# Performance work log

Hardware: AMD Instinct MI355X
Metric: run time of the kernel (lower is better)

The kernel has to match this reference:

```python
import jax, jax.numpy as jnp
import numpy as np

B, DIM, H, W, NH, WS = 128, 768, 16, 16, 12, 16
N = H * W  # 256, equals window_size**2


def setup_inputs() -> dict:
    key = jax.random.key(0)
    ks = jax.random.split(key, 8)
    s = 0.02  # small init scale for params
    return {
        "x": jax.random.normal(ks[0], (B, DIM, H, W), dtype=jnp.float32),
        "face_priors": jax.random.uniform(ks[1], (B, N, N), dtype=jnp.float32),
        "qkv_w": jax.random.normal(ks[2], (3 * DIM, DIM), dtype=jnp.float32) * s,
        "qkv_b": jax.random.normal(ks[3], (3 * DIM,), dtype=jnp.float32) * s,
        "rel_table": jax.random.normal(ks[4], ((2 * WS - 1) * (2 * WS - 1), NH), dtype=jnp.float32) * s,
        "face_prior": jax.random.normal(ks[5], (1, NH, N, N), dtype=jnp.float32) * s,
        "proj_w": jax.random.normal(ks[6], (DIM, DIM), dtype=jnp.float32) * s,
        "proj_b": jax.random.normal(ks[7], (DIM,), dtype=jnp.float32) * s,
    }


def _relative_position_bias(rel_table, h, w):
    # Static index computation (h, w are Python ints under jit).
    coords = jnp.stack(jnp.meshgrid(jnp.arange(h), jnp.arange(w), indexing="ij"))  # [2,h,w]
    flat = coords.reshape(2, -1)                     # [2, N]
    rel = flat[:, :, None] - flat[:, None, :]        # [2, N, N]
    idx = (rel[0] + h - 1) * (2 * w - 1) + (rel[1] + w - 1)  # [N, N]
    return rel_table[idx].transpose(2, 0, 1)         # [nh, N, N]


def reference(x, face_priors, qkv_w, qkv_b, rel_table, face_prior, proj_w, proj_b):
    b, c, h, w = x.shape
    n = h * w
    nh = face_prior.shape[1]
    hd = c // nh
    scale = hd ** -0.5

    x_flat = x.reshape(b, c, n).transpose(0, 2, 1)   # [B, N, C]
    qkv = (x_flat @ qkv_w.T + qkv_b).reshape(b, n, 3, nh, hd).transpose(2, 0, 3, 1, 4)
    q, k, v = qkv[0], qkv[1], qkv[2]                 # each [B, nh, N, hd]

    attn = jnp.einsum("bhnd,bhmd->bhnm", q, k) * scale
    attn = attn + face_prior + _relative_position_bias(rel_table, h, w)[None]
    attn = attn * face_priors[:, None]               # broadcast over heads
    attn = jax.nn.softmax(attn, axis=-1)

    out = jnp.einsum("bhnm,bhmd->bhnd", attn, v)     # [B, nh, N, hd]
    out = out.transpose(0, 2, 1, 3).reshape(b, n, c)
    out = out @ proj_w.T + proj_b                    # [B, N, C]
    return out.transpose(0, 2, 1).reshape(b, c, h, w)
```

## Files before the change

kernel.cpp:

```cpp
#include <hip/hip_runtime.h>

#define B_   128
#define DIM_ 768
#define NH_  12
#define HD_  64
#define N_   256

using half8 = __attribute__((ext_vector_type(8))) _Float16;
using half4 = __attribute__((ext_vector_type(4))) _Float16;
using f32x4 = __attribute__((ext_vector_type(4))) float;
typedef unsigned short u16;
typedef unsigned int   u32;

#define GLDS16(srcp, dstp) \
    __builtin_amdgcn_global_load_lds( \
        (const __attribute__((address_space(1))) void*)(srcp), \
        (__attribute__((address_space(3))) void*)(dstp), 16, 0, 0)

__device__ __forceinline__ int xcd_chunked(int orig, int nwg) {
    int xcd = orig & 7, loc = orig >> 3;
    int qq = nwg >> 3, rr = nwg & 7;
    return (xcd < rr ? xcd * (qq + 1) : rr * (qq + 1) + (xcd - rr) * qq) + loc;
}

__global__ __launch_bounds__(256) void bias16_kernel(
    const float* __restrict__ face_prior, const float* __restrict__ rel_table,
    _Float16* __restrict__ b16)
{
    int gid = blockIdx.x * 256 + threadIdx.x;
    int idx = gid * 2;
    union { _Float16 s[2]; u32 u; } P;
    #pragma unroll
    for (int j = 0; j < 2; ++j) {
        int id = idx + j;
        int m = id & 255;
        int n = (id >> 8) & 255;
        int h = id >> 16;
        int rn = n >> 4, cn = n & 15;
        int rm = m >> 4, cm = m & 15;
        int ridx = (rn - rm + 15) * 31 + (cn - cm + 15);
        P.s[j] = (_Float16)(face_prior[id] + rel_table[ridx * NH_ + h]);
    }
    *(u32*)(b16 + idx) = P.u;
}

__global__ __launch_bounds__(256) void conv_f32_f16(
    const float* __restrict__ in, _Float16* __restrict__ o16, int n8)
{
    int i = blockIdx.x * 256 + threadIdx.x;
    if (i >= n8) return;
    float4 a = *(const float4*)(in + (size_t)i * 8);
    float4 b = *(const float4*)(in + (size_t)i * 8 + 4);
    float v[8] = {a.x, a.y, a.z, a.w, b.x, b.y, b.z, b.w};
    union { _Float16 s[8]; uint4 q; } H;
    #pragma unroll
    for (int j = 0; j < 8; ++j) H.s[j] = (_Float16)v[j];
    *(uint4*)(o16 + (size_t)i * 8) = H.q;
}

__global__ __launch_bounds__(256) void conv_w_f16_staged(
    const float* __restrict__ in, _Float16* __restrict__ o16, int nchunk)
{
    int gid = blockIdx.x * 256 + threadIdx.x;
    if (gid >= nchunk) return;
    int t   = gid / 12288;
    int rem = gid % 12288;
    int ks  = rem >> 9;
    int c   = rem & 511;
    int mtb = c >> 6, kgrp = (c >> 4) & 3, r16 = c & 15;
    int srow = t * 128 + mtb * 16 + r16;
    int sk   = ks * 32 + kgrp * 8;
    float4 a = *(const float4*)(in + (size_t)srow * DIM_ + sk);
    float4 b = *(const float4*)(in + (size_t)srow * DIM_ + sk + 4);
    float v[8] = {a.x, a.y, a.z, a.w, b.x, b.y, b.z, b.w};
    union { _Float16 s[8]; uint4 q; } H;
    #pragma unroll
    for (int j = 0; j < 8; ++j) H.s[j] = (_Float16)v[j];
    *(uint4*)(o16 + (size_t)gid * 8) = H.q;
}

__global__ __launch_bounds__(256) void conv_qw_staged(
    const float* __restrict__ in, _Float16* __restrict__ o16, int nchunk)
{
    int gid = blockIdx.x * 256 + threadIdx.x;
    if (gid >= nchunk) return;
    int t   = gid / 24576;
    int rem = gid % 24576;
    int ks  = rem >> 10;
    int c   = rem & 1023;
    int mtb = c >> 6, kg = (c >> 4) & 3, r16 = c & 15;
    int srow = t * 256 + mtb * 16 + r16;
    int sk   = ks * 32 + kg * 8;
    float4 a = *(const float4*)(in + (size_t)srow * DIM_ + sk);
    float4 b = *(const float4*)(in + (size_t)srow * DIM_ + sk + 4);
    float v[8] = {a.x, a.y, a.z, a.w, b.x, b.y, b.z, b.w};
    union { _Float16 s[8]; uint4 q; } H;
    #pragma unroll
    for (int j = 0; j < 8; ++j) H.s[j] = (_Float16)v[j];
    *(uint4*)(o16 + (size_t)gid * 8) = H.q;
}

__global__ __launch_bounds__(256) void conv_transpose_x_f16(
    const float* __restrict__ x, _Float16* __restrict__ xa)
{
    __shared__ float T[64][65];
    const int b = blockIdx.z, k0 = blockIdx.x * 64, n0 = blockIdx.y * 64;
    const int t = threadIdx.x;
    const float* xb = x + (size_t)b * DIM_ * N_;
    {
        int nn = t & 63, kg = t >> 6;
        #pragma unroll
        for (int r = 0; r < 16; ++r) {
            int kk = r * 4 + kg;
            T[kk][nn] = xb[(size_t)(k0 + kk) * N_ + n0 + nn];
        }
    }
    __syncthreads();
    {
        int kk2 = (t & 31) * 2, ng = t >> 5;
        #pragma unroll
        for (int r = 0; r < 8; ++r) {
            int nn = r * 8 + ng;
            union { _Float16 s[2]; u32 u; } P;
            P.s[0] = (_Float16)T[kk2][nn];
            P.s[1] = (_Float16)T[kk2 + 1][nn];
            int n = n0 + nn, k = k0 + kk2;
            int ks = k >> 5, kg = (k >> 3) & 3, koff = k & 7;
            int mtb = n >> 4, r16 = n & 15;
            size_t o = (((size_t)b * 24 + ks) * 1024
                        + mtb * 64 + kg * 16 + r16) * 8 + koff;
            *(u32*)(xa + o) = P.u;
        }
    }
}

__global__ __launch_bounds__(512) void qkv_gemm(
    const _Float16* __restrict__ w16, const _Float16* __restrict__ x16,
    const float* __restrict__ bvec,
    _Float16* __restrict__ q16, _Float16* __restrict__ k16,
    _Float16* __restrict__ v16,
    int b0, int cb)
{
    extern __shared__ _Float16 lds[];

    const int tid  = threadIdx.x;
    const int lane = tid & 63;
    const int wv   = tid >> 6;
    const int wr   = wv >> 2;
    const int wc   = wv & 3;

    const int wg = xcd_chunked(blockIdx.x, cb * 9);
    const int by = wg % 9;
    const int bl = wg / 9;
    const int b  = b0 + bl;

    const _Float16* wbase = w16 + (size_t)by * 24 * 8192;
    const _Float16* xbase = x16 + (size_t)b  * 24 * 8192;

    f32x4 acc[8][4];
    #pragma unroll
    for (int i = 0; i < 8; ++i)
        #pragma unroll
        for (int j = 0; j < 4; ++j)
            acc[i][j] = (f32x4){0.f, 0.f, 0.f, 0.f};

    const int sb = wv * 512;

#define SGA(u, s, j) GLDS16(wbase + (size_t)(u) * 16384 + (j) * 4096 + sb + lane * 8, \
                            lds + (s) * 16384 + (j) * 4096 + sb)
#define SGB(u, s, j) GLDS16(xbase + (size_t)(u) * 16384 + (j) * 4096 + sb + lane * 8, \
                            lds + 32768 + (s) * 16384 + (j) * 4096 + sb)

    SGA(0, 0, 0); SGA(0, 0, 1); SGA(0, 0, 2); SGA(0, 0, 3);
    SGB(0, 0, 0); SGB(0, 0, 1); SGB(0, 0, 2); SGB(0, 0, 3);
    SGA(1, 1, 0); SGA(1, 1, 1); SGA(1, 1, 2); SGA(1, 1, 3);
    SGB(1, 1, 0); SGB(1, 1, 1); SGB(1, 1, 2); SGB(1, 1, 3);

    for (int u = 0; u < 12; ++u) {
        const int sl = u & 1;
        if (u < 11) asm volatile("s_waitcnt vmcnt(8)" ::: "memory");
        else        asm volatile("s_waitcnt vmcnt(0)" ::: "memory");
        __builtin_amdgcn_s_barrier();
        __builtin_amdgcn_sched_barrier(0);

        const _Float16* SA = lds + sl * 16384;
        const _Float16* SB = lds + 32768 + sl * 16384;

        half8 af[8][2];
        #pragma unroll
        for (int mt = 0; mt < 8; ++mt) {
            af[mt][0] = *(const half8*)&SA[((wr * 8 + mt) * 64 + lane) * 8];
            af[mt][1] = *(const half8*)&SA[8192 + ((wr * 8 + mt) * 64 + lane) * 8];
        }

        const bool pre = (u + 2 < 12);
        #pragma unroll
        for (int nt = 0; nt < 4; ++nt) {
            if (nt == 1 && pre) { SGA(u + 2, sl, 0); SGA(u + 2, sl, 1); }
            if (nt == 2 && pre) { SGA(u + 2, sl, 2); SGA(u + 2, sl, 3); }
            half8 bf0 = *(const half8*)&SB[((wc * 4 + nt) * 64 + lane) * 8];
            half8 bf1 = *(const half8*)&SB[8192 + ((wc * 4 + nt) * 64 + lane) * 8];
            __builtin_amdgcn_s_setprio(1);
            #pragma unroll
            for (int mt = 0; mt < 8; ++mt) {
                acc[mt][nt] = __builtin_amdgcn_mfma_f32_16x16x32_f16(af[mt][0], bf0, acc[mt][nt], 0, 0, 0);
                acc[mt][nt] = __builtin_amdgcn_mfma_f32_16x16x32_f16(af[mt][1], bf1, acc[mt][nt], 0, 0, 0);
            }
            __builtin_amdgcn_s_setprio(0);
            __builtin_amdgcn_s_barrier();
        }
        if (pre) { SGB(u + 2, sl, 0); SGB(u + 2, sl, 1); SGB(u + 2, sl, 2); SGB(u + 2, sl, 3); }
    }
#undef SGA
#undef SGB

    const int which = by / 3;
    _Float16* slab = (which == 0) ? q16 : (which == 1) ? k16 : v16;
    const int ocr0 = (by % 3) * 256 + wr * 128 + ((lane >> 4) << 2);
    const int nb   = wc * 64 + (lane & 15);

    #pragma unroll
    for (int mt = 0; mt < 8; ++mt) {
        int oc_in = ocr0 + mt * 16;
        float4 bv = *(const float4*)(bvec + which * DIM_ + oc_in);
        int hh = oc_in >> 6, d = oc_in & 63;
        size_t rowbase = ((size_t)bl * NH_ + hh) * (size_t)(N_ * HD_) + d;
        #pragma unroll
        for (int nt = 0; nt < 4; ++nt) {
            int n = nb + nt * 16;
            union { _Float16 s[4]; uint2 u; } H;
            H.s[0] = (_Float16)(acc[mt][nt][0] + bv.x);
            H.s[1] = (_Float16)(acc[mt][nt][1] + bv.y);
            H.s[2] = (_Float16)(acc[mt][nt][2] + bv.z);
            H.s[3] = (_Float16)(acc[mt][nt][3] + bv.w);
            *(uint2*)(slab + rowbase + (size_t)n * HD_) = H.u;
        }
    }
}

__global__ __launch_bounds__(256) void attn_mfma(
    const _Float16* __restrict__ q16, const _Float16* __restrict__ k16,
    const _Float16* __restrict__ v16,
    const _Float16* __restrict__ bias16, const _Float16* __restrict__ fpri16,
    _Float16* __restrict__ ao,
    int b0, int cb)
{
    extern __shared__ _Float16 ldsh[];
    _Float16* KL  = ldsh;
    _Float16* VtL = ldsh + 16384;
    const int tid  = threadIdx.x;
    const int lane = tid & 63;
    const int wv   = tid >> 6;
    _Float16* PL = ldsh + 32768 + wv * 512;

    const int bh = xcd_chunked(blockIdx.x, cb * NH_);
    const int bl = bh / NH_, h = bh % NH_;
    const int b  = b0 + bl;
    const size_t base = ((size_t)bl * NH_ + h) * (size_t)(N_ * HD_);

    const int l15 = lane & 15;
    const int lg  = lane >> 4;
    const int e   = (l15 & 3) << 1;

    #pragma unroll
    for (int s = 0; s < 8; ++s) {
        int idx = tid + s * 256;
        int r = idx >> 3, kc = (idx & 7) * 8;
        *(half8*)&KL[r * 64 + (kc ^ ((r & 7) << 3))] =
            *(const half8*)(k16 + base + (size_t)r * 64 + kc);
    }
    #pragma unroll
    for (int s = 0; s < 8; ++s) {
        int idx = tid + s * 256;
        int d = idx & 63, kkc = (idx >> 6) * 8;
        union { _Float16 sv[8]; half8 v; } t;
        #pragma unroll
        for (int j = 0; j < 8; ++j)
            t.sv[j] = v16[base + (size_t)(kkc + j) * 64 + d];
        *(half8*)&VtL[d * 256 + (kkc ^ ((d & 7) << 3))] = t.v;
    }
    __syncthreads();

    for (int qt = 0; qt < 4; ++qt) {
        const int qg = wv * 64 + qt * 16 + l15;
        const size_t qrow = base + (size_t)qg * 64;
        half8 bq[2];
        #pragma unroll
        for (int c = 0; c < 2; ++c)
            bq[c] = *(const half8*)(q16 + qrow + lg * 8 + c * 32);

        const _Float16* brow = bias16 + ((size_t)h * N_ + qg) * N_;
        const _Float16* frow = fpri16 + ((size_t)b * N_ + qg) * N_;

        float mrun = -1e30f, lrun = 0.f;
        f32x4 oacc[4];
        #pragma unroll
        for (int dt = 0; dt < 4; ++dt) oacc[dt] = (f32x4){0.f, 0.f, 0.f, 0.f};

        for (int ch = 0; ch < 2; ++ch) {
            f32x4 sacc[8];
            #pragma unroll
            for (int kt = 0; kt < 8; ++kt) {
                f32x4 sa = (f32x4){0.f, 0.f, 0.f, 0.f};
                int kr = ch * 128 + kt * 16 + l15;
                #pragma unroll
                for (int c = 0; c < 2; ++c) {
                    int kc = lg * 8 + c * 32;
                    half8 ah = *(const half8*)&KL[kr * 64 + (kc ^ ((kr & 7) << 3))];
                    sa = __builtin_amdgcn_mfma_f32_16x16x32_f16(ah, bq[c], sa, 0, 0, 0);
                }
                half4 bsv = *(const half4*)(brow + ch * 128 + kt * 16 + lg * 4);
                half4 fsv = *(const half4*)(frow + ch * 128 + kt * 16 + lg * 4);
                sacc[kt][0] = (sa[0] * 0.125f + (float)bsv[0]) * (float)fsv[0];
                sacc[kt][1] = (sa[1] * 0.125f + (float)bsv[1]) * (float)fsv[1];
                sacc[kt][2] = (sa[2] * 0.125f + (float)bsv[2]) * (float)fsv[2];
                sacc[kt][3] = (sa[3] * 0.125f + (float)bsv[3]) * (float)fsv[3];
            }

            float cmax = -1e30f;
            #pragma unroll
            for (int kt = 0; kt < 8; ++kt)
                cmax = fmaxf(cmax, fmaxf(fmaxf(sacc[kt][0], sacc[kt][1]),
                                         fmaxf(sacc[kt][2], sacc[kt][3])));
            cmax = fmaxf(cmax, __shfl_xor(cmax, 16));
            cmax = fmaxf(cmax, __shfl_xor(cmax, 32));
            float mnew = fmaxf(mrun, cmax);
            float corr = __expf(mrun - mnew);
            mrun = mnew;
            float csum = 0.f;
            #pragma unroll
            for (int kt = 0; kt < 8; ++kt) {
                #pragma unroll
                for (int j = 0; j < 4; ++j) {
                    float p = __expf(sacc[kt][j] - mnew);
                    sacc[kt][j] = p;
                    csum += p;
                }
            }
            csum += __shfl_xor(csum, 16);
            csum += __shfl_xor(csum, 32);
            lrun = lrun * corr + csum;
            #pragma unroll
            for (int dt = 0; dt < 4; ++dt) {
                oacc[dt][0] *= corr; oacc[dt][1] *= corr;
                oacc[dt][2] *= corr; oacc[dt][3] *= corr;
            }

            #pragma unroll
            for (int c2 = 0; c2 < 4; ++c2) {
                #pragma unroll
                for (int t = 0; t < 2; ++t) {
                    int kt = c2 * 2 + t;
                    union { _Float16 s[4]; uint2 u; } pw;
                    pw.s[0] = (_Float16)sacc[kt][0];
                    pw.s[1] = (_Float16)sacc[kt][1];
                    pw.s[2] = (_Float16)sacc[kt][2];
                    pw.s[3] = (_Float16)sacc[kt][3];
                    int u = (4 * t + lg) ^ e;
                    *(uint2*)&PL[l15 * 32 + u * 4] = pw.u;
                }
                half8 bp = *(const half8*)&PL[l15 * 32 + ((2 * lg) ^ e) * 4];
                int kc2 = ch * 128 + c2 * 32 + lg * 8;
                #pragma unroll
                for (int dt = 0; dt < 4; ++dt) {
                    int dr = dt * 16 + l15;
                    half8 av = *(const half8*)&VtL[dr * 256 + (kc2 ^ ((dr & 7) << 3))];
                    oacc[dt] = __builtin_amdgcn_mfma_f32_16x16x32_f16(av, bp, oacc[dt], 0, 0, 0);
                }
            }
        }

        float inv = 1.f / lrun;
        const int hf  = qg >> 7, mtb = (qg >> 4) & 7, r16 = qg & 15;
        #pragma unroll
        for (int dt = 0; dt < 4; ++dt) {
            int k = h * 64 + dt * 16 + lg * 4;
            int ks = k >> 5, kgrp = (k >> 3) & 3, koff = k & 7;
            size_t off = ((((size_t)(bl * 2 + hf) * 24 + ks) * 512)
                          + mtb * 64 + kgrp * 16 + r16) * 8 + koff;
            union { _Float16 s[4]; uint2 u; } H;
            #pragma unroll
            for (int j = 0; j < 4; ++j)
                H.s[j] = (_Float16)(oacc[dt][j] * inv);
            *(uint2*)(ao + off) = H.u;
        }
    }
}

__global__ __launch_bounds__(256) void proj_gemm(
    const _Float16* __restrict__ wst, const _Float16* __restrict__ ao,
    const float* __restrict__ bvec, float* __restrict__ outp,
    int b0, int cb)
{
    __shared__ __align__(16) _Float16 SW[4096], SX[4096];

    const int tid  = threadIdx.x;
    const int lane = tid & 63;
    const int wv   = tid >> 6;
    const int wr   = wv >> 1;
    const int wc   = wv & 1;

    const int wg = xcd_chunked(blockIdx.x, cb * 12);
    const int by = wg % 6;
    const int bx = wg / 6;
    const int bl = bx >> 1, half = bx & 1;
    const int b  = b0 + bl;

    const size_t wq0 = (size_t)by * 24 * 4096;
    const size_t xq0 = ((size_t)bl * 2 + half) * 24 * 4096;

    f32x4 acc[4][4];
    #pragma unroll
    for (int i = 0; i < 4; ++i)
        #pragma unroll
        for (int j = 0; j < 4; ++j)
            acc[i][j] = (f32x4){0.f, 0.f, 0.f, 0.f};

    const int d0 = wv * 512;

    for (int ks = 0; ks < 24; ++ks) {
        const size_t wq = wq0 + (size_t)ks * 4096 + d0;
        const size_t xq = xq0 + (size_t)ks * 4096 + d0;
        #pragma unroll
        for (int s = 0; s < 2; ++s) {
            GLDS16(wst + wq + s * 2048 + lane * 8, &SW[d0 + s * 2048]);
            GLDS16(ao  + xq + s * 2048 + lane * 8, &SX[d0 + s * 2048]);
        }
        __syncthreads();

        half8 ah[4];
        #pragma unroll
        for (int mt = 0; mt < 4; ++mt)
            ah[mt] = *(const half8*)&SW[((wr * 4 + mt) * 64 + lane) * 8];
        #pragma unroll
        for (int nt = 0; nt < 4; ++nt) {
            half8 bh = *(const half8*)&SX[((wc * 4 + nt) * 64 + lane) * 8];
            #pragma unroll
            for (int mt = 0; mt < 4; ++mt)
                acc[mt][nt] = __builtin_amdgcn_mfma_f32_16x16x32_f16(ah[mt], bh, acc[mt][nt], 0, 0, 0);
        }
        __syncthreads();
    }

    const int ocb = by * 128 + wr * 64 + (lane >> 4) * 4;
    const int nb  = half * 128 + wc * 64 + (lane & 15);

    #pragma unroll
    for (int mt = 0; mt < 4; ++mt) {
        int oc = ocb + mt * 16;
        float4 bv = *(const float4*)(bvec + oc);
        float* obase = outp + (size_t)b * DIM_ * N_ + (size_t)oc * N_;
        #pragma unroll
        for (int nt = 0; nt < 4; ++nt) {
            int n = nb + nt * 16;
            obase[0 * N_ + n] = acc[mt][nt][0] + bv.x;
            obase[1 * N_ + n] = acc[mt][nt][1] + bv.y;
            obase[2 * N_ + n] = acc[mt][nt][2] + bv.z;
            obase[3 * N_ + n] = acc[mt][nt][3] + bv.w;
        }
    }
}

extern "C" void kernel_launch(void* const* d_in, const int* in_sizes, int n_in,
                              void* d_out, int out_size, void* d_ws, size_t ws_size,
                              hipStream_t stream)
{
    const float* x           = (const float*)d_in[0];
    const float* face_priors = (const float*)d_in[1];
    const float* qkv_w       = (const float*)d_in[2];
    const float* qkv_b       = (const float*)d_in[3];
    const float* rel_table   = (const float*)d_in[4];
    const float* face_prior  = (const float*)d_in[5];
    const float* proj_w      = (const float*)d_in[6];
    const float* proj_b      = (const float*)d_in[7];
    float* out = (float*)d_out;

    _Float16* b16   = (_Float16*)d_ws;
    _Float16* fp16p = b16 + (size_t)NH_ * N_ * N_;
    _Float16* xa16  = fp16p + (size_t)B_ * N_ * N_;
    _Float16* qw16  = xa16 + (size_t)B_ * N_ * DIM_;
    _Float16* pw16  = qw16 + (size_t)3 * DIM_ * DIM_;
    _Float16* cbase = pw16 + (size_t)DIM_ * DIM_;

    const size_t PERSIST = 2ull * (NH_ * N_ * N_ + (size_t)B_ * N_ * N_
                         + (size_t)B_ * N_ * DIM_ + 4ull * DIM_ * DIM_);
    int CB = 1;
    const int cands[] = {128, 64, 32, 16, 8, 4, 2, 1};
    for (int ci = 0; ci < 8; ++ci) {
        if (PERSIST + (size_t)cands[ci] * 1572864ull <= ws_size) { CB = cands[ci]; break; }
    }
    const size_t SL = (size_t)CB * NH_ * N_ * HD_;
    _Float16* q16b = cbase;
    _Float16* k16b = q16b + SL;
    _Float16* v16b = k16b + SL;
    _Float16* aob  = v16b + SL;

    hipFuncSetAttribute((const void*)attn_mfma,
                        hipFuncAttributeMaxDynamicSharedMemorySize, 69632);
    hipFuncSetAttribute((const void*)qkv_gemm,
                        hipFuncAttributeMaxDynamicSharedMemorySize, 131072);

    bias16_kernel<<<(NH_ * N_ * N_ / 2) / 256, 256, 0, stream>>>(face_prior, rel_table, b16);
    conv_f32_f16<<<((B_ * N_ * N_ / 8) + 255) / 256, 256, 0, stream>>>(face_priors, fp16p, B_ * N_ * N_ / 8);
    conv_qw_staged<<<(9 * 24576 + 255) / 256, 256, 0, stream>>>(qkv_w, qw16, 9 * 24576);
    conv_w_f16_staged<<<(6 * 12288 + 255) / 256, 256, 0, stream>>>(proj_w, pw16, 6 * 12288);
    conv_transpose_x_f16<<<dim3(12, 4, B_), 256, 0, stream>>>(x, xa16);

    for (int b0 = 0; b0 < B_; b0 += CB) {
        qkv_gemm<<<CB * 9, 512, 131072, stream>>>(
            qw16, xa16, qkv_b, q16b, k16b, v16b, b0, CB);

        attn_mfma<<<CB * NH_, 256, 69632, stream>>>(
            q16b, k16b, v16b, b16, fp16p, aob, b0, CB);

        proj_gemm<<<CB * 12, 256, 0, stream>>>(
            pw16, aob, proj_b, out, b0, CB);
    }
}
```

Before: 389.7 us.

## Pre-permute bias and face-prior tensors into MFMA fragment order, add setprio around MFMAs

The fp16 bias and face-prior tensors are now written in the exact order each attention wavefront reads them, so every lane's half4 load becomes one contiguous 512-byte wave access instead of strided row reads. The preprocessing kernels change to emit this permuted layout. s_setprio hints are also placed around the MFMA blocks to favour matrix issue across waves. The fp32 face-prior reads in the prep kernel become strided by row, and the gather is otherwise unchanged.

```diff
diff --git a/kernel.cpp b/kernel.cpp
--- a/kernel.cpp
+++ b/kernel.cpp
@@ -23,39 +23,43 @@
     return (xcd < rr ? xcd * (qq + 1) : rr * (qq + 1) + (xcd - rr) * qq) + loc;
 }
 
-__global__ __launch_bounds__(256) void bias16_kernel(
+__global__ __launch_bounds__(256) void bias16p_kernel(
     const float* __restrict__ face_prior, const float* __restrict__ rel_table,
-    _Float16* __restrict__ b16)
-{
-    int gid = blockIdx.x * 256 + threadIdx.x;
-    int idx = gid * 2;
-    union { _Float16 s[2]; u32 u; } P;
-    #pragma unroll
-    for (int j = 0; j < 2; ++j) {
-        int id = idx + j;
-        int m = id & 255;
-        int n = (id >> 8) & 255;
-        int h = id >> 16;
+    _Float16* __restrict__ b16p)
+{
+    int g = blockIdx.x * 256 + threadIdx.x;
+    int lane = g & 63;
+    int kt = (g >> 6) & 7, ch = (g >> 9) & 1, qt = (g >> 10) & 3;
+    int wv = (g >> 12) & 3, h = g >> 14;
+    int qg  = wv * 64 + qt * 16 + (lane & 15);
+    int kk0 = ch * 128 + kt * 16 + ((lane >> 4) << 2);
+    union { _Float16 s[4]; uint2 u; } P;
+    #pragma unroll
+    for (int j = 0; j < 4; ++j) {
+        int m = kk0 + j, n = qg;
         int rn = n >> 4, cn = n & 15;
         int rm = m >> 4, cm = m & 15;
         int ridx = (rn - rm + 15) * 31 + (cn - cm + 15);
-        P.s[j] = (_Float16)(face_prior[id] + rel_table[ridx * NH_ + h]);
-    }
-    *(u32*)(b16 + idx) = P.u;
-}
-
-__global__ __launch_bounds__(256) void conv_f32_f16(
-    const float* __restrict__ in, _Float16* __restrict__ o16, int n8)
-{
-    int i = blockIdx.x * 256 + threadIdx.x;
-    if (i >= n8) return;
-    float4 a = *(const float4*)(in + (size_t)i * 8);
-    float4 b = *(const float4*)(in + (size_t)i * 8 + 4);
-    float v[8] = {a.x, a.y, a.z, a.w, b.x, b.y, b.z, b.w};
-    union { _Float16 s[8]; uint4 q; } H;
-    #pragma unroll
-    for (int j = 0; j < 8; ++j) H.s[j] = (_Float16)v[j];
-    *(uint4*)(o16 + (size_t)i * 8) = H.q;
+        P.s[j] = (_Float16)(face_prior[((size_t)h * N_ + n) * N_ + m]
+                            + rel_table[ridx * NH_ + h]);
+    }
+    *(uint2*)(b16p + (size_t)g * 4) = P.u;
+}
+
+__global__ __launch_bounds__(256) void fpri16p_kernel(
+    const float* __restrict__ fpri, _Float16* __restrict__ f16p)
+{
+    int g = blockIdx.x * 256 + threadIdx.x;
+    int lane = g & 63;
+    int kt = (g >> 6) & 7, ch = (g >> 9) & 1, qt = (g >> 10) & 3;
+    int wv = (g >> 12) & 3, b = g >> 14;
+    int qg  = wv * 64 + qt * 16 + (lane & 15);
+    int kk0 = ch * 128 + kt * 16 + ((lane >> 4) << 2);
+    float4 v = *(const float4*)(fpri + ((size_t)b * N_ + qg) * N_ + kk0);
+    union { _Float16 s[4]; uint2 u; } P;
+    P.s[0] = (_Float16)v.x; P.s[1] = (_Float16)v.y;
+    P.s[2] = (_Float16)v.z; P.s[3] = (_Float16)v.w;
+    *(uint2*)(f16p + (size_t)g * 4) = P.u;
 }
 
 __global__ __launch_bounds__(256) void conv_w_f16_staged(
@@ -241,7 +245,7 @@
 __global__ __launch_bounds__(256) void attn_mfma(
     const _Float16* __restrict__ q16, const _Float16* __restrict__ k16,
     const _Float16* __restrict__ v16,
-    const _Float16* __restrict__ bias16, const _Float16* __restrict__ fpri16,
+    const _Float16* __restrict__ b16p, const _Float16* __restrict__ f16p,
     _Float16* __restrict__ ao,
     int b0, int cb)
 {
@@ -262,6 +266,9 @@
     const int lg  = lane >> 4;
     const int e   = (l15 & 3) << 1;
 
+    const _Float16* bpw = b16p + (size_t)h * 65536 + (size_t)wv * 16384;
+    const _Float16* fpw = f16p + (size_t)b * 65536 + (size_t)wv * 16384;
+
     #pragma unroll
     for (int s = 0; s < 8; ++s) {
         int idx = tid + s * 256;
@@ -289,9 +296,6 @@
         for (int c = 0; c < 2; ++c)
             bq[c] = *(const half8*)(q16 + qrow + lg * 8 + c * 32);
 
-        const _Float16* brow = bias16 + ((size_t)h * N_ + qg) * N_;
-        const _Float16* frow = fpri16 + ((size_t)b * N_ + qg) * N_;
-
         float mrun = -1e30f, lrun = 0.f;
         f32x4 oacc[4];
         #pragma unroll
@@ -303,14 +307,17 @@
             for (int kt = 0; kt < 8; ++kt) {
                 f32x4 sa = (f32x4){0.f, 0.f, 0.f, 0.f};
                 int kr = ch * 128 + kt * 16 + l15;
+                __builtin_amdgcn_s_setprio(1);
                 #pragma unroll
                 for (int c = 0; c < 2; ++c) {
                     int kc = lg * 8 + c * 32;
                     half8 ah = *(const half8*)&KL[kr * 64 + (kc ^ ((kr & 7) << 3))];
                     sa = __builtin_amdgcn_mfma_f32_16x16x32_f16(ah, bq[c], sa, 0, 0, 0);
                 }
-                half4 bsv = *(const half4*)(brow + ch * 128 + kt * 16 + lg * 4);
-                half4 fsv = *(const half4*)(frow + ch * 128 + kt * 16 + lg * 4);
+                __builtin_amdgcn_s_setprio(0);
+                int poff = (((qt * 2 + ch) * 8 + kt) << 8) + (lane << 2);
+                half4 bsv = *(const half4*)(bpw + poff);
+                half4 fsv = *(const half4*)(fpw + poff);
                 sacc[kt][0] = (sa[0] * 0.125f + (float)bsv[0]) * (float)fsv[0];
                 sacc[kt][1] = (sa[1] * 0.125f + (float)bsv[1]) * (float)fsv[1];
                 sacc[kt][2] = (sa[2] * 0.125f + (float)bsv[2]) * (float)fsv[2];
@@ -361,12 +368,14 @@
                 }
                 half8 bp = *(const half8*)&PL[l15 * 32 + ((2 * lg) ^ e) * 4];
                 int kc2 = ch * 128 + c2 * 32 + lg * 8;
+                __builtin_amdgcn_s_setprio(1);
                 #pragma unroll
                 for (int dt = 0; dt < 4; ++dt) {
                     int dr = dt * 16 + l15;
                     half8 av = *(const half8*)&VtL[dr * 256 + (kc2 ^ ((dr & 7) << 3))];
                     oacc[dt] = __builtin_amdgcn_mfma_f32_16x16x32_f16(av, bp, oacc[dt], 0, 0, 0);
                 }
+                __builtin_amdgcn_s_setprio(0);
             }
         }
 
@@ -475,9 +484,9 @@
     const float* proj_b      = (const float*)d_in[7];
     float* out = (float*)d_out;
 
-    _Float16* b16   = (_Float16*)d_ws;
-    _Float16* fp16p = b16 + (size_t)NH_ * N_ * N_;
-    _Float16* xa16  = fp16p + (size_t)B_ * N_ * N_;
+    _Float16* b16p  = (_Float16*)d_ws;
+    _Float16* f16p  = b16p + (size_t)NH_ * N_ * N_;
+    _Float16* xa16  = f16p + (size_t)B_ * N_ * N_;
     _Float16* qw16  = xa16 + (size_t)B_ * N_ * DIM_;
     _Float16* pw16  = qw16 + (size_t)3 * DIM_ * DIM_;
     _Float16* cbase = pw16 + (size_t)DIM_ * DIM_;
@@ -500,8 +509,8 @@
     hipFuncSetAttribute((const void*)qkv_gemm,
                         hipFuncAttributeMaxDynamicSharedMemorySize, 131072);
 
-    bias16_kernel<<<(NH_ * N_ * N_ / 2) / 256, 256, 0, stream>>>(face_prior, rel_table, b16);
-    conv_f32_f16<<<((B_ * N_ * N_ / 8) + 255) / 256, 256, 0, stream>>>(face_priors, fp16p, B_ * N_ * N_ / 8);
+    bias16p_kernel<<<(NH_ * N_ * N_ / 4) / 256, 256, 0, stream>>>(face_prior, rel_table, b16p);
+    fpri16p_kernel<<<(B_ * N_ * N_ / 4) / 256, 256, 0, stream>>>(face_priors, f16p);
     conv_qw_staged<<<(9 * 24576 + 255) / 256, 256, 0, stream>>>(qkv_w, qw16, 9 * 24576);
     conv_w_f16_staged<<<(6 * 12288 + 255) / 256, 256, 0, stream>>>(proj_w, pw16, 6 * 12288);
     conv_transpose_x_f16<<<dim3(12, 4, B_), 256, 0, stream>>>(x, xa16);
@@ -511,7 +520,7 @@
             qw16, xa16, qkv_b, q16b, k16b, v16b, b0, CB);
 
         attn_mfma<<<CB * NH_, 256, 69632, stream>>>(
-            q16b, k16b, v16b, b16, fp16p, aob, b0, CB);
+            q16b, k16b, v16b, b16p, f16p, aob, b0, CB);
 
         proj_gemm<<<CB * 12, 256, 0, stream>>>(
             pw16, aob, proj_b, out, b0, CB);
```

Result: slower. 408.5 us (+4.8%).
